# Kernel optimization log

Hardware: AMD Instinct MI355X
Metric: run time of the kernel (lower is better)

The kernel has to match this reference:

```python
import jax, jax.numpy as jnp
import numpy as np

DIM = 512
DIM_TIME = 64
DIM_FF = 2048
B, L = 2, 512
EPS = 1e-5


def _layer_norm(x, g, b):
    mu = jnp.mean(x, axis=-1, keepdims=True)
    var = jnp.mean((x - mu) ** 2, axis=-1, keepdims=True)
    return (x - mu) * jax.lax.rsqrt(var + EPS) * g + b


def _sioconv(u, wa, hid_re, hid_im):
    # u: (B, L, Dt) float. Faithful to the FFT/triu construction, expressed as
    # cumulative log-sums (linear conv with all-ones == causal cumsum).
    Bb, Ll, Dt = u.shape
    out = (u @ wa.T).reshape(Bb, Ll, Dt, 2)          # linear_a, view_as_complex
    a_sqr = out[..., 0] ** 2 + out[..., 1] ** 2
    a = (out[..., 0] + 1j * out[..., 1]) * (jax.lax.rsqrt(a_sqr) * jnp.exp(-a_sqr))
    a = jnp.transpose(a, (0, 2, 1))                  # (B, Dt, L)
    a_ln = jnp.log(a)
    S = jnp.cumsum(a_ln, axis=-1)                    # S_k = sum_{j<=k} ln a_j
    S_prev = jnp.concatenate([jnp.zeros_like(S[..., :1]), S[..., :-1]], axis=-1)
    # c[b,d,i,k] = exp(S_k - S_{i-1}) = prod_{j=i..k} a_j, kept for k >= i-1
    diff = S[:, :, None, :] - S_prev[:, :, :, None]  # (B, Dt, L, L)
    idx = jnp.arange(Ll)
    mask = idx[None, :] >= (idx[:, None] - 1)        # k >= i-1 (triu diag=-1)
    c = jnp.where(mask, jnp.exp(diff), 0.0)
    uc = jnp.transpose(u.astype(jnp.complex64), (0, 2, 1))   # (B, Dt, L)
    hidden = (hid_re + 1j * hid_im)[None, :] * jnp.ones((Bb, 1), jnp.complex64)
    xin = jnp.concatenate([hidden[..., None], uc[..., :-1]], axis=-1)  # rolled + h0
    h = jnp.einsum('bdik,bdk->bdi', c, xin)
    h = h.at[:, :, -1].add(uc[:, :, -1])
    return jnp.transpose(h.real, (0, 2, 1)).astype(u.dtype)


def _ffn(x, w1, b1, w2, b2):
    return jax.nn.silu(x @ w1.T + b1) @ w2.T + b2


def setup_inputs() -> dict:
    key = jax.random.key(0)
    ks = jax.random.split(key, 12)
    d, dt, dff = DIM, DIM_TIME, DIM_FF
    return {
        'x': jax.random.normal(ks[0], (B, L, d), jnp.float32),
        'ln1_g': jnp.ones((d,), jnp.float32), 'ln1_b': jnp.zeros((d,), jnp.float32),
        'fc_w': jax.random.normal(ks[1], (dt, d), jnp.float32) * d ** -0.5,
        'fc_b': jnp.zeros((dt,), jnp.float32),
        'lin_in_w': jax.random.normal(ks[2], (dt, d), jnp.float32) * d ** -0.5,
        'lin_in_b': jnp.zeros((dt,), jnp.float32),
        'wa': jax.random.normal(ks[3], (2 * dt, dt), jnp.float32) * dt ** -0.5,
        'hid_re': jax.random.normal(ks[4], (dt,), jnp.float32),
        'hid_im': jax.random.normal(ks[5], (dt,), jnp.float32),
        'lin_out_w': jax.random.normal(ks[6], (d, dt), jnp.float32) * dt ** -0.5,
        'lin_out_b': jnp.zeros((d,), jnp.float32),
        'ln2_g': jnp.ones((d,), jnp.float32), 'ln2_b': jnp.zeros((d,), jnp.float32),
        'w1': jax.random.normal(ks[7], (dff, d), jnp.float32) * d ** -0.5,
        'b1': jnp.zeros((dff,), jnp.float32),
        'w2': jax.random.normal(ks[8], (d, dff), jnp.float32) * dff ** -0.5,
        'b2': jnp.zeros((d,), jnp.float32),
    }


def reference(x, ln1_g, ln1_b, fc_w, fc_b, lin_in_w, lin_in_b, wa, hid_re, hid_im,
              lin_out_w, lin_out_b, ln2_g, ln2_b, w1, b1, w2, b2):
    x_res = x
    xn = _layer_norm(x, ln1_g, ln1_b)
    y = jax.nn.silu(xn @ fc_w.T + fc_b)                  # gate, (B, L, Dt)
    u = xn @ lin_in_w.T + lin_in_b                       # (B, L, Dt)
    h = _sioconv(u, wa, hid_re, hid_im)
    x = (h * y) @ lin_out_w.T + lin_out_b + x_res        # dropout = identity (eval)
    x_res = x
    x = _ffn(_layer_norm(x, ln2_g, ln2_b), w1, b1, w2, b2) + x_res
    return x
```

## Files before the change

### kernel.cpp

```cpp
#include <hip/hip_runtime.h>
#include <math.h>

#define LSEQ 512
#define DMODEL 512
#define DT 64
#define DFF 2048

typedef unsigned short u16;
typedef __attribute__((ext_vector_type(8))) short short8;
typedef __attribute__((ext_vector_type(4))) float f32x4;
typedef __attribute__((ext_vector_type(16))) float f32x16;

__device__ __forceinline__ float wave_sum(float v) {
#pragma unroll
  for (int o = 32; o > 0; o >>= 1) v += __shfl_xor(v, o, 64);
  return v;
}

__device__ __forceinline__ u16 f2bf(float f) {
  unsigned int u = __float_as_uint(f);
  u += 0x7fffu + ((u >> 16) & 1u);
  return (u16)(u >> 16);
}
__device__ __forceinline__ float bf2f(u16 h) {
  return __uint_as_float(((unsigned int)h) << 16);
}
__device__ __forceinline__ void splitbf(float f, u16& h, u16& l) {
  h = f2bf(f);
  l = f2bf(f - bf2f(h));
}


__global__ __launch_bounds__(256) void k_pre(
    const float* __restrict__ w1, const float* __restrict__ w2,
    const float* __restrict__ fcw, const float* __restrict__ liw,
    const float* __restrict__ wa, const float* __restrict__ low,
    const float* __restrict__ x, const float* __restrict__ g1,
    const float* __restrict__ be1,
    u16* __restrict__ w1s, u16* __restrict__ w2s,
    u16* __restrict__ fclh, u16* __restrict__ fcll,
    u16* __restrict__ wah, u16* __restrict__ wal,
    u16* __restrict__ lowh, u16* __restrict__ lowl,
    u16* __restrict__ xnh, u16* __restrict__ xnl)
{
  if (blockIdx.x >= 2152) {
    const int lane = threadIdx.x & 63, wv = threadIdx.x >> 6;
    const int row = (blockIdx.x - 2152) * 4 + wv;
    const float* xr = x + (size_t)row * DMODEL;
    float v[8]; float s = 0.f;
#pragma unroll
    for (int j = 0; j < 8; ++j) { v[j] = xr[lane + 64 * j]; s += v[j]; }
    s = wave_sum(s);
    const float mu = s * (1.f / 512.f);
    float q = 0.f;
#pragma unroll
    for (int j = 0; j < 8; ++j) { float dd = v[j] - mu; q += dd * dd; }
    q = wave_sum(q);
    const float rstd = rsqrtf(q * (1.f / 512.f) + 1e-5f);
#pragma unroll
    for (int j = 0; j < 8; ++j) {
      int idx = lane + 64 * j;
      float o = (v[j] - mu) * rstd * g1[idx] + be1[idx];
      u16 h, l; splitbf(o, h, l);
      xnh[(size_t)row * DMODEL + idx] = h;
      xnl[(size_t)row * DMODEL + idx] = l;
    }
    return;
  }
  int i = blockIdx.x * 256 + threadIdx.x;
  if (i >= 550912) return;
  if (i < 262144) {
    int r = i >> 7, c0 = (i & 127) << 2;
    float4 v = ((const float4*)w1)[i];
    ushort4 o;
    o.x = f2bf(v.x); o.y = f2bf(v.y); o.z = f2bf(v.z); o.w = f2bf(v.w);
    int lane = (r & 31) + (((c0 & 15) >> 3) << 5);
    int flat = (r >> 5) * 16384 + (c0 >> 4) * 512 + lane * 8 + (c0 & 7);
    *(ushort4*)(w1s + flat) = o;
    return;
  }
  if (i < 524288) {
    int ii = i - 262144;
    int r = ii >> 9, c0 = (ii & 511) << 2;
    float4 v = ((const float4*)w2)[ii];
    ushort4 o;
    o.x = f2bf(v.x); o.y = f2bf(v.y); o.z = f2bf(v.z); o.w = f2bf(v.w);
    int lane = (r & 31) + (((c0 & 15) >> 3) << 5);
    int flat = (r >> 5) * 65536 + (c0 >> 4) * 512 + lane * 8 + (c0 & 7);
    *(ushort4*)(w2s + flat) = o;
    return;
  }
  const float* s; int j; u16 *dh, *dl;
  if (i < 532480)      { s = fcw; j = i - 524288;        dh = fclh; dl = fcll; }
  else if (i < 540672) { s = liw; j = i - 532480 + 8192; dh = fclh; dl = fcll; }
  else if (i < 542720) { s = wa;  j = i - 540672;        dh = wah;  dl = wal;  }
  else                 { s = low; j = i - 542720;        dh = lowh; dl = lowl; }
  int soff = (i < 532480) ? i - 524288 :
             (i < 540672) ? i - 532480 :
             (i < 542720) ? i - 540672 : i - 542720;
  float4 v = ((const float4*)s)[soff];
  ushort4 oh, ol;
  splitbf(v.x, oh.x, ol.x); splitbf(v.y, oh.y, ol.y);
  splitbf(v.z, oh.z, ol.z); splitbf(v.w, oh.w, ol.w);
  ((ushort4*)dh)[j] = oh;
  ((ushort4*)dl)[j] = ol;
}

__global__ __launch_bounds__(512) void k_fa(
    const u16* __restrict__ xnh, const u16* __restrict__ xnl,
    const u16* __restrict__ fclh, const u16* __restrict__ fcll,
    const u16* __restrict__ wah, const u16* __restrict__ wal,
    const float* __restrict__ fcb, const float* __restrict__ lib,
    float* __restrict__ y_o, float* __restrict__ u_o,
    float* __restrict__ ar_o, float* __restrict__ ai_o)
{
  __shared__ __align__(16) u16 ush[16][80];
  __shared__ __align__(16) u16 usl[16][80];
  const int w = threadIdx.x >> 6, lane = threadIdx.x & 63;
  const int mt = blockIdx.x;
  const int lr = lane & 15, lk = lane >> 4;

  {
    const size_t aoff = (size_t)(mt * 16 + lr) * DMODEL + lk * 8;
    const size_t boff = (size_t)(w * 16 + lr) * DMODEL + lk * 8;
    f32x4 acc = {};
#pragma unroll 4
    for (int k = 0; k < DMODEL; k += 32) {
      short8 ah = *(const short8*)(xnh + aoff + k);
      short8 al = *(const short8*)(xnl + aoff + k);
      short8 bh = *(const short8*)(fclh + boff + k);
      short8 bl = *(const short8*)(fcll + boff + k);
      acc = __builtin_amdgcn_mfma_f32_16x16x32_bf16(ah, bh, acc, 0, 0, 0);
      acc = __builtin_amdgcn_mfma_f32_16x16x32_bf16(ah, bl, acc, 0, 0, 0);
      acc = __builtin_amdgcn_mfma_f32_16x16x32_bf16(al, bh, acc, 0, 0, 0);
    }
    const int c = w * 16 + lr;
#pragma unroll
    for (int j = 0; j < 4; ++j) {
      int rl = lk * 4 + j;
      int row = mt * 16 + rl;
      float v = acc[j];
      if (c < DT) {
        v += fcb[c];
        y_o[row * DT + c] = v / (1.f + expf(-v));
      } else {
        int d = c - DT;
        v += lib[d];
        u_o[row * DT + d] = v;
        u16 h, l; splitbf(v, h, l);
        ush[rl][d] = h; usl[rl][d] = l;
      }
    }
  }
  __syncthreads();
  {
    const size_t boff = (size_t)(w * 16 + lr) * DT + lk * 8;
    f32x4 acc = {};
#pragma unroll
    for (int ks = 0; ks < 2; ++ks) {
      short8 ah = *(const short8*)&ush[lr][ks * 32 + lk * 8];
      short8 al = *(const short8*)&usl[lr][ks * 32 + lk * 8];
      short8 bh = *(const short8*)(wah + boff + ks * 32);
      short8 bl = *(const short8*)(wal + boff + ks * 32);
      acc = __builtin_amdgcn_mfma_f32_16x16x32_bf16(ah, bh, acc, 0, 0, 0);
      acc = __builtin_amdgcn_mfma_f32_16x16x32_bf16(ah, bl, acc, 0, 0, 0);
      acc = __builtin_amdgcn_mfma_f32_16x16x32_bf16(al, bh, acc, 0, 0, 0);
    }
    const int c = w * 16 + lr;
#pragma unroll
    for (int j = 0; j < 4; ++j) {
      float v = acc[j];
      float p = __shfl_xor(v, 1, 64);
      float re = (lane & 1) ? p : v;
      float im = (lane & 1) ? v : p;
      float asq = re * re + im * im;
      float sc = rsqrtf(asq) * expf(-asq);
      int row = mt * 16 + lk * 4 + j;
      int d = c >> 1;
      if (lane & 1) ai_o[row * DT + d] = im * sc;
      else          ar_o[row * DT + d] = re * sc;
    }
  }
}

__global__ __launch_bounds__(64) void k_scan2(
    const float* __restrict__ u, const float* __restrict__ ar, const float* __restrict__ ai,
    const float* __restrict__ hr, const float* __restrict__ hi, float* __restrict__ h_o)
{
  const int blk = blockIdx.x;
  const int b = blk >> 6, d = blk & 63;
  const int lane = threadIdx.x;
  const size_t base = (size_t)b * LSEQ * DT + d;
  const int i0 = lane * 8;

  float a_r[8], a_i[8], b_r[8], b_i[8];
#pragma unroll
  for (int e = 0; e < 8; ++e) {
    int i = i0 + e;
    a_r[e] = ar[base + (size_t)i * DT];
    a_i[e] = ai[base + (size_t)i * DT];
    if (i >= 2)      { b_r[e] = u[base + (size_t)(i - 2) * DT]; b_i[e] = 0.f; }
    else if (i == 1) { b_r[e] = hr[d]; b_i[e] = hi[d]; }
    else             { b_r[e] = 0.f;   b_i[e] = 0.f; }
  }

  float Ar = 1.f, Ai = 0.f, Br = 0.f, Bi = 0.f;
#pragma unroll
  for (int e = 0; e < 8; ++e) {
    float nBr = fmaf(Ar, b_r[e], fmaf(-Ai, b_i[e], Br));
    float nBi = fmaf(Ar, b_i[e], fmaf( Ai, b_r[e], Bi));
    float nAr = Ar * a_r[e] - Ai * a_i[e];
    float nAi = Ar * a_i[e] + Ai * a_r[e];
    Ar = nAr; Ai = nAi; Br = nBr; Bi = nBi;
  }

#pragma unroll
  for (int dlt = 1; dlt < 64; dlt <<= 1) {
    float Ar2 = __shfl_down(Ar, dlt, 64);
    float Ai2 = __shfl_down(Ai, dlt, 64);
    float Br2 = __shfl_down(Br, dlt, 64);
    float Bi2 = __shfl_down(Bi, dlt, 64);
    if (lane + dlt < 64) {
      float nAr = Ar * Ar2 - Ai * Ai2;
      float nAi = Ar * Ai2 + Ai * Ar2;
      float nBr = fmaf(Ar, Br2, fmaf(-Ai, Bi2, Br));
      float nBi = fmaf(Ar, Bi2, fmaf( Ai, Br2, Bi));
      Ar = nAr; Ai = nAi; Br = nBr; Bi = nBi;
    }
  }

  float A1r = __shfl_down(Ar, 1, 64), A1i = __shfl_down(Ai, 1, 64);
  float B1r = __shfl_down(Br, 1, 64), B1i = __shfl_down(Bi, 1, 64);
  if (lane == 63) { A1r = 1.f; A1i = 0.f; B1r = 0.f; B1i = 0.f; }
  const float r512 = u[base + (size_t)(LSEQ - 2) * DT];
  float rr = fmaf(A1r, r512, B1r);
  float ri = fmaf(A1i, r512, B1i);

  const float uL = u[base + (size_t)(LSEQ - 1) * DT];
#pragma unroll
  for (int e = 7; e >= 0; --e) {
    int i = i0 + e;
    float nr = fmaf(a_r[e], rr, fmaf(-a_i[e], ri, b_r[e]));
    float ni = fmaf(a_r[e], ri, fmaf( a_i[e], rr, b_i[e]));
    rr = nr; ri = ni;
    float outv = rr;
    if (i == LSEQ - 1) outv += uL;
    h_o[base + (size_t)i * DT] = outv;
  }
}

__global__ __launch_bounds__(1024) void k_midln(
    const float* __restrict__ h, const float* __restrict__ y,
    const u16* __restrict__ lowh, const u16* __restrict__ lowl,
    const float* __restrict__ lob, const float* __restrict__ x,
    const float* __restrict__ g2, const float* __restrict__ be2,
    float* __restrict__ x2_o, u16* __restrict__ xn2s)
{
  __shared__ __align__(16) u16 hyh[16][80];
  __shared__ __align__(16) u16 hyl[16][80];
  __shared__ float x2s[16][520];
  const int tid = threadIdx.x;
  const int w = tid >> 6, lane = tid & 63;
  const int lr = lane & 15, lk = lane >> 4;
  const int mt = blockIdx.x;

  {
    int r = tid >> 6, d = tid & 63;
    int row = mt * 16 + r;
    float v = h[row * DT + d] * y[row * DT + d];
    u16 hh, ll; splitbf(v, hh, ll);
    hyh[r][d] = hh; hyl[r][d] = ll;
  }
  __syncthreads();

#pragma unroll
  for (int t = 0; t < 2; ++t) {
    const int nt = w * 2 + t;
    const size_t boff = (size_t)(nt * 16 + lr) * DT + lk * 8;
    f32x4 acc = {};
#pragma unroll
    for (int ks = 0; ks < 2; ++ks) {
      short8 ah = *(const short8*)&hyh[lr][ks * 32 + lk * 8];
      short8 al = *(const short8*)&hyl[lr][ks * 32 + lk * 8];
      short8 bh = *(const short8*)(lowh + boff + ks * 32);
      short8 bl = *(const short8*)(lowl + boff + ks * 32);
      acc = __builtin_amdgcn_mfma_f32_16x16x32_bf16(ah, bh, acc, 0, 0, 0);
      acc = __builtin_amdgcn_mfma_f32_16x16x32_bf16(ah, bl, acc, 0, 0, 0);
      acc = __builtin_amdgcn_mfma_f32_16x16x32_bf16(al, bh, acc, 0, 0, 0);
    }
    const int c = nt * 16 + lr;
#pragma unroll
    for (int j = 0; j < 4; ++j) {
      int rl = lk * 4 + j;
      int row = mt * 16 + rl;
      float v = acc[j] + lob[c] + x[(size_t)row * DMODEL + c];
      x2s[rl][c] = v;
      x2_o[(size_t)row * DMODEL + c] = v;
    }
  }
  __syncthreads();

  {
    const int r = w;
    const int row = mt * 16 + r;
    float v[8]; float s = 0.f;
#pragma unroll
    for (int j = 0; j < 8; ++j) { v[j] = x2s[r][lane + 64 * j]; s += v[j]; }
    s = wave_sum(s);
    const float mu = s * (1.f / 512.f);
    float q = 0.f;
#pragma unroll
    for (int j = 0; j < 8; ++j) { float dd = v[j] - mu; q += dd * dd; }
    q = wave_sum(q);
    const float rstd = rsqrtf(q * (1.f / 512.f) + 1e-5f);
    const int t32 = row >> 5, r32 = row & 31;
#pragma unroll
    for (int j = 0; j < 8; ++j) {
      int idx = lane + 64 * j;
      float o = (v[j] - mu) * rstd * g2[idx] + be2[idx];
      int lane_s = r32 + (((idx & 15) >> 3) << 5);
      xn2s[t32 * 16384 + (idx >> 4) * 512 + lane_s * 8 + (idx & 7)] = f2bf(o);
    }
  }
}

__global__ __launch_bounds__(256) void k_ffn1(
    const u16* __restrict__ As, const u16* __restrict__ Bs,
    const float* __restrict__ bias, u16* __restrict__ Cs)
{
  const int w = threadIdx.x >> 6, lane = threadIdx.x & 63;
  const int mt = blockIdx.x, nt = blockIdx.y * 4 + w;
  const u16* a = As + mt * 16384 + lane * 8;
  const u16* b = Bs + nt * 16384 + lane * 8;
  f32x16 acc = {};
#pragma unroll 8
  for (int kb = 0; kb < 32; ++kb)
    acc = __builtin_amdgcn_mfma_f32_32x32x16_bf16(*(const short8*)(a + kb * 512),
                                                  *(const short8*)(b + kb * 512),
                                                  acc, 0, 0, 0);
  const int l31 = lane & 31, hi = lane >> 5;
  const int col = nt * 32 + l31;
  const float bb = bias[col];
  const int kb_c = col >> 4;
  const int half_c = (col & 15) >> 3, e_c = col & 7;
#pragma unroll
  for (int r = 0; r < 16; ++r) {
    int row32 = (r & 3) + 8 * (r >> 2) + 4 * hi;
    float v = acc[r] + bb;
    v = v / (1.f + expf(-v));
    int lane_s = row32 + (half_c << 5);
    Cs[mt * 65536 + kb_c * 512 + lane_s * 8 + e_c] = f2bf(v);
  }
}

__global__ __launch_bounds__(256) void k_ffn2(
    const u16* __restrict__ As, const u16* __restrict__ Bs,
    const float* __restrict__ b2, const float* __restrict__ x2,
    float* __restrict__ out)
{
  __shared__ float red[4][16][64];
  const int w = threadIdx.x >> 6, lane = threadIdx.x & 63;
  const int mt = blockIdx.x, nt = blockIdx.y;
  const u16* a = As + mt * 65536 + w * 32 * 512 + lane * 8;
  const u16* b = Bs + nt * 65536 + w * 32 * 512 + lane * 8;
  f32x16 acc = {};
#pragma unroll 8
  for (int kb = 0; kb < 32; ++kb)
    acc = __builtin_amdgcn_mfma_f32_32x32x16_bf16(*(const short8*)(a + kb * 512),
                                                  *(const short8*)(b + kb * 512),
                                                  acc, 0, 0, 0);
#pragma unroll
  for (int r = 0; r < 16; ++r) red[w][r][lane] = acc[r];
  __syncthreads();
  for (int s = threadIdx.x; s < 1024; s += 256) {
    int r = s >> 6, l = s & 63;
    float v = red[0][r][l] + red[1][r][l] + red[2][r][l] + red[3][r][l];
    int row = mt * 32 + (r & 3) + 8 * (r >> 2) + 4 * (l >> 5);
    int col = nt * 32 + (l & 31);
    out[(size_t)row * DMODEL + col] =
        v + b2[col] + x2[(size_t)row * DMODEL + col];
  }
}

extern "C" void kernel_launch(void* const* d_in, const int* in_sizes, int n_in,
                              void* d_out, int out_size, void* d_ws, size_t ws_size,
                              hipStream_t stream) {
  const float* x    = (const float*)d_in[0];
  const float* ln1g = (const float*)d_in[1];
  const float* ln1b = (const float*)d_in[2];
  const float* fcw  = (const float*)d_in[3];
  const float* fcb  = (const float*)d_in[4];
  const float* liw  = (const float*)d_in[5];
  const float* lib  = (const float*)d_in[6];
  const float* wa   = (const float*)d_in[7];
  const float* hidr = (const float*)d_in[8];
  const float* hidi = (const float*)d_in[9];
  const float* low  = (const float*)d_in[10];
  const float* lob  = (const float*)d_in[11];
  const float* ln2g = (const float*)d_in[12];
  const float* ln2b = (const float*)d_in[13];
  const float* w1   = (const float*)d_in[14];
  const float* b1   = (const float*)d_in[15];
  const float* w2   = (const float*)d_in[16];
  const float* b2   = (const float*)d_in[17];
  float* out = (float*)d_out;
  float* ws  = (float*)d_ws;

  float* y_   = ws;
  float* u_   = y_  + 65536;
  float* ar_  = u_  + 65536;
  float* ai_  = ar_ + 65536;
  float* h_   = ai_ + 65536;
  float* x2_  = h_  + 65536;
  u16* p = (u16*)(x2_ + 524288);
  u16* xnh  = p;            p += 524288;
  u16* xnl  = p;            p += 524288;
  u16* xn2s = p;            p += 524288;
  u16* h1s  = p;            p += 2097152;
  u16* w1s  = p;            p += 1048576;
  u16* w2s  = p;            p += 1048576;
  u16* fclh = p;            p += 65536;
  u16* fcll = p;            p += 65536;
  u16* wah  = p;            p += 8192;
  u16* wal  = p;            p += 8192;
  u16* lowh = p;            p += 32768;
  u16* lowl = p;            p += 32768;

  k_pre<<<2408, 256, 0, stream>>>(w1, w2, fcw, liw, wa, low, x, ln1g, ln1b,
                                  w1s, w2s, fclh, fcll, wah, wal, lowh, lowl,
                                  xnh, xnl);
  k_fa<<<64, 512, 0, stream>>>(xnh, xnl, fclh, fcll, wah, wal, fcb, lib,
                               y_, u_, ar_, ai_);
  k_scan2<<<128, 64, 0, stream>>>(u_, ar_, ai_, hidr, hidi, h_);
  k_midln<<<64, 1024, 0, stream>>>(h_, y_, lowh, lowl, lob, x, ln2g, ln2b,
                                   x2_, xn2s);
  k_ffn1<<<dim3(32, 16), 256, 0, stream>>>(xn2s, w1s, b1, h1s);
  k_ffn2<<<dim3(32, 16), 256, 0, stream>>>(h1s, w2s, b2, x2_, out);
}
```

Measured before the change: 62.86 us.

## Fuse all six kernels into one cooperative persistent kernel with grid syncs

Replaces the six separate launches (weight prep/LN1, gate+a projection, scan, out-proj+LN2, FFN1, FFN2) with a single cooperative kernel of 256 blocks of 512 threads. Stages are separated by grid-wide syncs, and per-stage shared memory is overlaid in a union. This removes the per-launch overhead and the inter-kernel gaps. In exchange, several stages now run on only a fraction of the grid (64 blocks or 128 waves), and each grid barrier has its own cost.

Result: slower. 222.9 us (+254.6%).

```diff
diff --git a/kernel.cpp b/kernel.cpp
--- a/kernel.cpp
+++ b/kernel.cpp
@@ -1,5 +1,8 @@
 #include <hip/hip_runtime.h>
+#include <hip/hip_cooperative_groups.h>
 #include <math.h>
+
+namespace cg = cooperative_groups;
 
 #define LSEQ 512
 #define DMODEL 512
@@ -31,21 +34,41 @@
 }
 
 
-__global__ __launch_bounds__(256) void k_pre(
+__global__ __launch_bounds__(512, 2) void k_mega(
     const float* __restrict__ w1, const float* __restrict__ w2,
     const float* __restrict__ fcw, const float* __restrict__ liw,
     const float* __restrict__ wa, const float* __restrict__ low,
     const float* __restrict__ x, const float* __restrict__ g1,
-    const float* __restrict__ be1,
+    const float* __restrict__ be1, const float* __restrict__ fcb,
+    const float* __restrict__ lib, const float* __restrict__ hidr,
+    const float* __restrict__ hidi, const float* __restrict__ lob,
+    const float* __restrict__ g2, const float* __restrict__ be2,
+    const float* __restrict__ b1, const float* __restrict__ b2,
+    float* __restrict__ y_, float* __restrict__ u_,
+    float* __restrict__ ar_, float* __restrict__ ai_,
+    float* __restrict__ h_, float* __restrict__ x2_,
+    u16* __restrict__ xnh, u16* __restrict__ xnl,
+    u16* __restrict__ xn2s, u16* __restrict__ h1s,
     u16* __restrict__ w1s, u16* __restrict__ w2s,
     u16* __restrict__ fclh, u16* __restrict__ fcll,
     u16* __restrict__ wah, u16* __restrict__ wal,
     u16* __restrict__ lowh, u16* __restrict__ lowl,
-    u16* __restrict__ xnh, u16* __restrict__ xnl)
+    float* __restrict__ out)
 {
-  if (blockIdx.x >= 2152) {
-    const int lane = threadIdx.x & 63, wv = threadIdx.x >> 6;
-    const int row = (blockIdx.x - 2152) * 4 + wv;
+  alignas(16) __shared__ union {
+    struct { u16 ush[16][80]; u16 usl[16][80]; } s1;
+    struct { u16 hyh[16][80]; u16 hyl[16][80]; float x2s[16][520]; } s3;
+    struct { float red[2][4][16][64]; } s5;
+  } sm;
+
+  cg::grid_group gg = cg::this_grid();
+  const int blk = blockIdx.x, tid = threadIdx.x;
+  const int wv = tid >> 6, lane = tid & 63;
+  const int gw = blk * 8 + wv;
+  const int lr = lane & 15, lk = lane >> 4;
+
+  if (gw < 1024) {
+    const int row = gw;
     const float* xr = x + (size_t)row * DMODEL;
     float v[8]; float s = 0.f;
 #pragma unroll
@@ -65,320 +88,282 @@
       xnh[(size_t)row * DMODEL + idx] = h;
       xnl[(size_t)row * DMODEL + idx] = l;
     }
-    return;
-  }
-  int i = blockIdx.x * 256 + threadIdx.x;
-  if (i >= 550912) return;
-  if (i < 262144) {
-    int r = i >> 7, c0 = (i & 127) << 2;
-    float4 v = ((const float4*)w1)[i];
-    ushort4 o;
-    o.x = f2bf(v.x); o.y = f2bf(v.y); o.z = f2bf(v.z); o.w = f2bf(v.w);
-    int lane = (r & 31) + (((c0 & 15) >> 3) << 5);
-    int flat = (r >> 5) * 16384 + (c0 >> 4) * 512 + lane * 8 + (c0 & 7);
-    *(ushort4*)(w1s + flat) = o;
-    return;
-  }
-  if (i < 524288) {
-    int ii = i - 262144;
-    int r = ii >> 9, c0 = (ii & 511) << 2;
-    float4 v = ((const float4*)w2)[ii];
-    ushort4 o;
-    o.x = f2bf(v.x); o.y = f2bf(v.y); o.z = f2bf(v.z); o.w = f2bf(v.w);
-    int lane = (r & 31) + (((c0 & 15) >> 3) << 5);
-    int flat = (r >> 5) * 65536 + (c0 >> 4) * 512 + lane * 8 + (c0 & 7);
-    *(ushort4*)(w2s + flat) = o;
-    return;
-  }
-  const float* s; int j; u16 *dh, *dl;
-  if (i < 532480)      { s = fcw; j = i - 524288;        dh = fclh; dl = fcll; }
-  else if (i < 540672) { s = liw; j = i - 532480 + 8192; dh = fclh; dl = fcll; }
-  else if (i < 542720) { s = wa;  j = i - 540672;        dh = wah;  dl = wal;  }
-  else                 { s = low; j = i - 542720;        dh = lowh; dl = lowl; }
-  int soff = (i < 532480) ? i - 524288 :
-             (i < 540672) ? i - 532480 :
-             (i < 542720) ? i - 540672 : i - 542720;
-  float4 v = ((const float4*)s)[soff];
-  ushort4 oh, ol;
-  splitbf(v.x, oh.x, ol.x); splitbf(v.y, oh.y, ol.y);
-  splitbf(v.z, oh.z, ol.z); splitbf(v.w, oh.w, ol.w);
-  ((ushort4*)dh)[j] = oh;
-  ((ushort4*)dl)[j] = ol;
-}
-
-__global__ __launch_bounds__(512) void k_fa(
-    const u16* __restrict__ xnh, const u16* __restrict__ xnl,
-    const u16* __restrict__ fclh, const u16* __restrict__ fcll,
-    const u16* __restrict__ wah, const u16* __restrict__ wal,
-    const float* __restrict__ fcb, const float* __restrict__ lib,
-    float* __restrict__ y_o, float* __restrict__ u_o,
-    float* __restrict__ ar_o, float* __restrict__ ai_o)
-{
-  __shared__ __align__(16) u16 ush[16][80];
-  __shared__ __align__(16) u16 usl[16][80];
-  const int w = threadIdx.x >> 6, lane = threadIdx.x & 63;
-  const int mt = blockIdx.x;
-  const int lr = lane & 15, lk = lane >> 4;
+  }
+  for (int i = blk * 512 + tid; i < 550912; i += 131072) {
+    if (i < 262144) {
+      int r = i >> 7, c0 = (i & 127) << 2;
+      float4 v = ((const float4*)w1)[i];
+      ushort4 o;
+      o.x = f2bf(v.x); o.y = f2bf(v.y); o.z = f2bf(v.z); o.w = f2bf(v.w);
+      int lane_s = (r & 31) + (((c0 & 15) >> 3) << 5);
+      int flat = (r >> 5) * 16384 + (c0 >> 4) * 512 + lane_s * 8 + (c0 & 7);
+      *(ushort4*)(w1s + flat) = o;
+    } else if (i < 524288) {
+      int ii = i - 262144;
+      int r = ii >> 9, c0 = (ii & 511) << 2;
+      float4 v = ((const float4*)w2)[ii];
+      ushort4 o;
+      o.x = f2bf(v.x); o.y = f2bf(v.y); o.z = f2bf(v.z); o.w = f2bf(v.w);
+      int lane_s = (r & 31) + (((c0 & 15) >> 3) << 5);
+      int flat = (r >> 5) * 65536 + (c0 >> 4) * 512 + lane_s * 8 + (c0 & 7);
+      *(ushort4*)(w2s + flat) = o;
+    } else {
+      const float* s; int j; u16 *dh, *dl;
+      if (i < 532480)      { s = fcw; j = i - 524288;        dh = fclh; dl = fcll; }
+      else if (i < 540672) { s = liw; j = i - 532480 + 8192; dh = fclh; dl = fcll; }
+      else if (i < 542720) { s = wa;  j = i - 540672;        dh = wah;  dl = wal;  }
+      else                 { s = low; j = i - 542720;        dh = lowh; dl = lowl; }
+      int soff = (i < 532480) ? i - 524288 :
+                 (i < 540672) ? i - 532480 :
+                 (i < 542720) ? i - 540672 : i - 542720;
+      float4 v = ((const float4*)s)[soff];
+      ushort4 oh, ol;
+      splitbf(v.x, oh.x, ol.x); splitbf(v.y, oh.y, ol.y);
+      splitbf(v.z, oh.z, ol.z); splitbf(v.w, oh.w, ol.w);
+      ((ushort4*)dh)[j] = oh;
+      ((ushort4*)dl)[j] = ol;
+    }
+  }
+  gg.sync();
+
+  if (blk < 64) {
+    const int mt = blk;
+    {
+      const size_t aoff = (size_t)(mt * 16 + lr) * DMODEL + lk * 8;
+      const size_t boff = (size_t)(wv * 16 + lr) * DMODEL + lk * 8;
+      f32x4 acc = {};
+#pragma unroll 4
+      for (int k = 0; k < DMODEL; k += 32) {
+        short8 ah = *(const short8*)(xnh + aoff + k);
+        short8 al = *(const short8*)(xnl + aoff + k);
+        short8 bh = *(const short8*)(fclh + boff + k);
+        short8 bl = *(const short8*)(fcll + boff + k);
+        acc = __builtin_amdgcn_mfma_f32_16x16x32_bf16(ah, bh, acc, 0, 0, 0);
+        acc = __builtin_amdgcn_mfma_f32_16x16x32_bf16(ah, bl, acc, 0, 0, 0);
+        acc = __builtin_amdgcn_mfma_f32_16x16x32_bf16(al, bh, acc, 0, 0, 0);
+      }
+      const int c = wv * 16 + lr;
+#pragma unroll
+      for (int j = 0; j < 4; ++j) {
+        int rl = lk * 4 + j;
+        int row = mt * 16 + rl;
+        float v = acc[j];
+        if (c < DT) {
+          v += fcb[c];
+          y_[row * DT + c] = v / (1.f + expf(-v));
+        } else {
+          int d = c - DT;
+          v += lib[d];
+          u_[row * DT + d] = v;
+          u16 h, l; splitbf(v, h, l);
+          sm.s1.ush[rl][d] = h; sm.s1.usl[rl][d] = l;
+        }
+      }
+    }
+    __syncthreads();
+    {
+      const size_t boff = (size_t)(wv * 16 + lr) * DT + lk * 8;
+      f32x4 acc = {};
+#pragma unroll
+      for (int ks = 0; ks < 2; ++ks) {
+        short8 ah = *(const short8*)&sm.s1.ush[lr][ks * 32 + lk * 8];
+        short8 al = *(const short8*)&sm.s1.usl[lr][ks * 32 + lk * 8];
+        short8 bh = *(const short8*)(wah + boff + ks * 32);
+        short8 bl = *(const short8*)(wal + boff + ks * 32);
+        acc = __builtin_amdgcn_mfma_f32_16x16x32_bf16(ah, bh, acc, 0, 0, 0);
+        acc = __builtin_amdgcn_mfma_f32_16x16x32_bf16(ah, bl, acc, 0, 0, 0);
+        acc = __builtin_amdgcn_mfma_f32_16x16x32_bf16(al, bh, acc, 0, 0, 0);
+      }
+      const int c = wv * 16 + lr;
+#pragma unroll
+      for (int j = 0; j < 4; ++j) {
+        float v = acc[j];
+        float p = __shfl_xor(v, 1, 64);
+        float re = (lane & 1) ? p : v;
+        float im = (lane & 1) ? v : p;
+        float asq = re * re + im * im;
+        float sc = rsqrtf(asq) * expf(-asq);
+        int row = mt * 16 + lk * 4 + j;
+        int d = c >> 1;
+        if (lane & 1) ai_[row * DT + d] = im * sc;
+        else          ar_[row * DT + d] = re * sc;
+      }
+    }
+  }
+  gg.sync();
+
+  if (gw < 128) {
+    const int b = gw >> 6, d = gw & 63;
+    const size_t base = (size_t)b * LSEQ * DT + d;
+    const int i0 = lane * 8;
+    float a_r[8], a_i[8], b_r[8], b_i[8];
+#pragma unroll
+    for (int e = 0; e < 8; ++e) {
+      int i = i0 + e;
+      a_r[e] = ar_[base + (size_t)i * DT];
+      a_i[e] = ai_[base + (size_t)i * DT];
+      if (i >= 2)      { b_r[e] = u_[base + (size_t)(i - 2) * DT]; b_i[e] = 0.f; }
+      else if (i == 1) { b_r[e] = hidr[d]; b_i[e] = hidi[d]; }
+      else             { b_r[e] = 0.f;     b_i[e] = 0.f; }
+    }
+    float Ar = 1.f, Ai = 0.f, Br = 0.f, Bi = 0.f;
+#pragma unroll
+    for (int e = 0; e < 8; ++e) {
+      float nBr = fmaf(Ar, b_r[e], fmaf(-Ai, b_i[e], Br));
+      float nBi = fmaf(Ar, b_i[e], fmaf( Ai, b_r[e], Bi));
+      float nAr = Ar * a_r[e] - Ai * a_i[e];
+      float nAi = Ar * a_i[e] + Ai * a_r[e];
+      Ar = nAr; Ai = nAi; Br = nBr; Bi = nBi;
+    }
+#pragma unroll
+    for (int dlt = 1; dlt < 64; dlt <<= 1) {
+      float Ar2 = __shfl_down(Ar, dlt, 64);
+      float Ai2 = __shfl_down(Ai, dlt, 64);
+      float Br2 = __shfl_down(Br, dlt, 64);
+      float Bi2 = __shfl_down(Bi, dlt, 64);
+      if (lane + dlt < 64) {
+        float nAr = Ar * Ar2 - Ai * Ai2;
+        float nAi = Ar * Ai2 + Ai * Ar2;
+        float nBr = fmaf(Ar, Br2, fmaf(-Ai, Bi2, Br));
+        float nBi = fmaf(Ar, Bi2, fmaf( Ai, Br2, Bi));
+        Ar = nAr; Ai = nAi; Br = nBr; Bi = nBi;
+      }
+    }
+    float A1r = __shfl_down(Ar, 1, 64), A1i = __shfl_down(Ai, 1, 64);
+    float B1r = __shfl_down(Br, 1, 64), B1i = __shfl_down(Bi, 1, 64);
+    if (lane == 63) { A1r = 1.f; A1i = 0.f; B1r = 0.f; B1i = 0.f; }
+    const float r512 = u_[base + (size_t)(LSEQ - 2) * DT];
+    float rr = fmaf(A1r, r512, B1r);
+    float ri = fmaf(A1i, r512, B1i);
+    const float uL = u_[base + (size_t)(LSEQ - 1) * DT];
+#pragma unroll
+    for (int e = 7; e >= 0; --e) {
+      int i = i0 + e;
+      float nr = fmaf(a_r[e], rr, fmaf(-a_i[e], ri, b_r[e]));
+      float ni = fmaf(a_r[e], ri, fmaf( a_i[e], rr, b_i[e]));
+      rr = nr; ri = ni;
+      float outv = rr;
+      if (i == LSEQ - 1) outv += uL;
+      h_[base + (size_t)i * DT] = outv;
+    }
+  }
+  gg.sync();
+
+  if (blk < 64) {
+    const int mt = blk;
+#pragma unroll
+    for (int it = 0; it < 2; ++it) {
+      int idx = it * 512 + tid;
+      int r = idx >> 6, d = idx & 63;
+      int row = mt * 16 + r;
+      float v = h_[row * DT + d] * y_[row * DT + d];
+      u16 hh, ll; splitbf(v, hh, ll);
+      sm.s3.hyh[r][d] = hh; sm.s3.hyl[r][d] = ll;
+    }
+    __syncthreads();
+#pragma unroll
+    for (int t = 0; t < 4; ++t) {
+      const int nt = wv * 4 + t;
+      const size_t boff = (size_t)(nt * 16 + lr) * DT + lk * 8;
+      f32x4 acc = {};
+#pragma unroll
+      for (int ks = 0; ks < 2; ++ks) {
+        short8 ah = *(const short8*)&sm.s3.hyh[lr][ks * 32 + lk * 8];
+        short8 al = *(const short8*)&sm.s3.hyl[lr][ks * 32 + lk * 8];
+        short8 bh = *(const short8*)(lowh + boff + ks * 32);
+        short8 bl = *(const short8*)(lowl + boff + ks * 32);
+        acc = __builtin_amdgcn_mfma_f32_16x16x32_bf16(ah, bh, acc, 0, 0, 0);
+        acc = __builtin_amdgcn_mfma_f32_16x16x32_bf16(ah, bl, acc, 0, 0, 0);
+        acc = __builtin_amdgcn_mfma_f32_16x16x32_bf16(al, bh, acc, 0, 0, 0);
+      }
+      const int c = nt * 16 + lr;
+#pragma unroll
+      for (int j = 0; j < 4; ++j) {
+        int rl = lk * 4 + j;
+        int row = mt * 16 + rl;
+        float v = acc[j] + lob[c] + x[(size_t)row * DMODEL + c];
+        sm.s3.x2s[rl][c] = v;
+        x2_[(size_t)row * DMODEL + c] = v;
+      }
+    }
+    __syncthreads();
+#pragma unroll
+    for (int rr2 = 0; rr2 < 2; ++rr2) {
+      const int r = wv * 2 + rr2;
+      const int row = mt * 16 + r;
+      float v[8]; float s = 0.f;
+#pragma unroll
+      for (int j = 0; j < 8; ++j) { v[j] = sm.s3.x2s[r][lane + 64 * j]; s += v[j]; }
+      s = wave_sum(s);
+      const float mu = s * (1.f / 512.f);
+      float q = 0.f;
+#pragma unroll
+      for (int j = 0; j < 8; ++j) { float dd = v[j] - mu; q += dd * dd; }
+      q = wave_sum(q);
+      const float rstd = rsqrtf(q * (1.f / 512.f) + 1e-5f);
+      const int t32 = row >> 5, r32 = row & 31;
+#pragma unroll
+      for (int j = 0; j < 8; ++j) {
+        int idx = lane + 64 * j;
+        float o = (v[j] - mu) * rstd * g2[idx] + be2[idx];
+        int lane_s = r32 + (((idx & 15) >> 3) << 5);
+        xn2s[t32 * 16384 + (idx >> 4) * 512 + lane_s * 8 + (idx & 7)] = f2bf(o);
+      }
+    }
+  }
+  gg.sync();
 
   {
-    const size_t aoff = (size_t)(mt * 16 + lr) * DMODEL + lk * 8;
-    const size_t boff = (size_t)(w * 16 + lr) * DMODEL + lk * 8;
-    f32x4 acc = {};
-#pragma unroll 4
-    for (int k = 0; k < DMODEL; k += 32) {
-      short8 ah = *(const short8*)(xnh + aoff + k);
-      short8 al = *(const short8*)(xnl + aoff + k);
-      short8 bh = *(const short8*)(fclh + boff + k);
-      short8 bl = *(const short8*)(fcll + boff + k);
-      acc = __builtin_amdgcn_mfma_f32_16x16x32_bf16(ah, bh, acc, 0, 0, 0);
-      acc = __builtin_amdgcn_mfma_f32_16x16x32_bf16(ah, bl, acc, 0, 0, 0);
-      acc = __builtin_amdgcn_mfma_f32_16x16x32_bf16(al, bh, acc, 0, 0, 0);
-    }
-    const int c = w * 16 + lr;
-#pragma unroll
-    for (int j = 0; j < 4; ++j) {
-      int rl = lk * 4 + j;
-      int row = mt * 16 + rl;
-      float v = acc[j];
-      if (c < DT) {
-        v += fcb[c];
-        y_o[row * DT + c] = v / (1.f + expf(-v));
-      } else {
-        int d = c - DT;
-        v += lib[d];
-        u_o[row * DT + d] = v;
-        u16 h, l; splitbf(v, h, l);
-        ush[rl][d] = h; usl[rl][d] = l;
-      }
-    }
-  }
-  __syncthreads();
+    const int mt = gw & 31, nt = gw >> 5;
+    const u16* a = xn2s + mt * 16384 + lane * 8;
+    const u16* b = w1s + nt * 16384 + lane * 8;
+    f32x16 acc = {};
+#pragma unroll 8
+    for (int kb = 0; kb < 32; ++kb)
+      acc = __builtin_amdgcn_mfma_f32_32x32x16_bf16(*(const short8*)(a + kb * 512),
+                                                    *(const short8*)(b + kb * 512),
+                                                    acc, 0, 0, 0);
+    const int l31 = lane & 31, hi = lane >> 5;
+    const int col = nt * 32 + l31;
+    const float bb = b1[col];
+    const int kb_c = col >> 4;
+    const int half_c = (col & 15) >> 3, e_c = col & 7;
+#pragma unroll
+    for (int r = 0; r < 16; ++r) {
+      int row32 = (r & 3) + 8 * (r >> 2) + 4 * hi;
+      float v = acc[r] + bb;
+      v = v / (1.f + expf(-v));
+      int lane_s = row32 + (half_c << 5);
+      h1s[mt * 65536 + kb_c * 512 + lane_s * 8 + e_c] = f2bf(v);
+    }
+  }
+  gg.sync();
+
   {
-    const size_t boff = (size_t)(w * 16 + lr) * DT + lk * 8;
-    f32x4 acc = {};
-#pragma unroll
-    for (int ks = 0; ks < 2; ++ks) {
-      short8 ah = *(const short8*)&ush[lr][ks * 32 + lk * 8];
-      short8 al = *(const short8*)&usl[lr][ks * 32 + lk * 8];
-      short8 bh = *(const short8*)(wah + boff + ks * 32);
-      short8 bl = *(const short8*)(wal + boff + ks * 32);
-      acc = __builtin_amdgcn_mfma_f32_16x16x32_bf16(ah, bh, acc, 0, 0, 0);
-      acc = __builtin_amdgcn_mfma_f32_16x16x32_bf16(ah, bl, acc, 0, 0, 0);
-      acc = __builtin_amdgcn_mfma_f32_16x16x32_bf16(al, bh, acc, 0, 0, 0);
-    }
-    const int c = w * 16 + lr;
-#pragma unroll
-    for (int j = 0; j < 4; ++j) {
-      float v = acc[j];
-      float p = __shfl_xor(v, 1, 64);
-      float re = (lane & 1) ? p : v;
-      float im = (lane & 1) ? v : p;
-      float asq = re * re + im * im;
-      float sc = rsqrtf(asq) * expf(-asq);
-      int row = mt * 16 + lk * 4 + j;
-      int d = c >> 1;
-      if (lane & 1) ai_o[row * DT + d] = im * sc;
-      else          ar_o[row * DT + d] = re * sc;
-    }
-  }
-}
-
-__global__ __launch_bounds__(64) void k_scan2(
-    const float* __restrict__ u, const float* __restrict__ ar, const float* __restrict__ ai,
-    const float* __restrict__ hr, const float* __restrict__ hi, float* __restrict__ h_o)
-{
-  const int blk = blockIdx.x;
-  const int b = blk >> 6, d = blk & 63;
-  const int lane = threadIdx.x;
-  const size_t base = (size_t)b * LSEQ * DT + d;
-  const int i0 = lane * 8;
-
-  float a_r[8], a_i[8], b_r[8], b_i[8];
-#pragma unroll
-  for (int e = 0; e < 8; ++e) {
-    int i = i0 + e;
-    a_r[e] = ar[base + (size_t)i * DT];
-    a_i[e] = ai[base + (size_t)i * DT];
-    if (i >= 2)      { b_r[e] = u[base + (size_t)(i - 2) * DT]; b_i[e] = 0.f; }
-    else if (i == 1) { b_r[e] = hr[d]; b_i[e] = hi[d]; }
-    else             { b_r[e] = 0.f;   b_i[e] = 0.f; }
-  }
-
-  float Ar = 1.f, Ai = 0.f, Br = 0.f, Bi = 0.f;
-#pragma unroll
-  for (int e = 0; e < 8; ++e) {
-    float nBr = fmaf(Ar, b_r[e], fmaf(-Ai, b_i[e], Br));
-    float nBi = fmaf(Ar, b_i[e], fmaf( Ai, b_r[e], Bi));
-    float nAr = Ar * a_r[e] - Ai * a_i[e];
-    float nAi = Ar * a_i[e] + Ai * a_r[e];
-    Ar = nAr; Ai = nAi; Br = nBr; Bi = nBi;
-  }
-
-#pragma unroll
-  for (int dlt = 1; dlt < 64; dlt <<= 1) {
-    float Ar2 = __shfl_down(Ar, dlt, 64);
-    float Ai2 = __shfl_down(Ai, dlt, 64);
-    float Br2 = __shfl_down(Br, dlt, 64);
-    float Bi2 = __shfl_down(Bi, dlt, 64);
-    if (lane + dlt < 64) {
-      float nAr = Ar * Ar2 - Ai * Ai2;
-      float nAi = Ar * Ai2 + Ai * Ar2;
-      float nBr = fmaf(Ar, Br2, fmaf(-Ai, Bi2, Br));
-      float nBi = fmaf(Ar, Bi2, fmaf( Ai, Br2, Bi));
-      Ar = nAr; Ai = nAi; Br = nBr; Bi = nBi;
-    }
-  }
-
-  float A1r = __shfl_down(Ar, 1, 64), A1i = __shfl_down(Ai, 1, 64);
-  float B1r = __shfl_down(Br, 1, 64), B1i = __shfl_down(Bi, 1, 64);
-  if (lane == 63) { A1r = 1.f; A1i = 0.f; B1r = 0.f; B1i = 0.f; }
-  const float r512 = u[base + (size_t)(LSEQ - 2) * DT];
-  float rr = fmaf(A1r, r512, B1r);
-  float ri = fmaf(A1i, r512, B1i);
-
-  const float uL = u[base + (size_t)(LSEQ - 1) * DT];
-#pragma unroll
-  for (int e = 7; e >= 0; --e) {
-    int i = i0 + e;
-    float nr = fmaf(a_r[e], rr, fmaf(-a_i[e], ri, b_r[e]));
-    float ni = fmaf(a_r[e], ri, fmaf( a_i[e], rr, b_i[e]));
-    rr = nr; ri = ni;
-    float outv = rr;
-    if (i == LSEQ - 1) outv += uL;
-    h_o[base + (size_t)i * DT] = outv;
-  }
-}
-
-__global__ __launch_bounds__(1024) void k_midln(
-    const float* __restrict__ h, const float* __restrict__ y,
-    const u16* __restrict__ lowh, const u16* __restrict__ lowl,
-    const float* __restrict__ lob, const float* __restrict__ x,
-    const float* __restrict__ g2, const float* __restrict__ be2,
-    float* __restrict__ x2_o, u16* __restrict__ xn2s)
-{
-  __shared__ __align__(16) u16 hyh[16][80];
-  __shared__ __align__(16) u16 hyl[16][80];
-  __shared__ float x2s[16][520];
-  const int tid = threadIdx.x;
-  const int w = tid >> 6, lane = tid & 63;
-  const int lr = lane & 15, lk = lane >> 4;
-  const int mt = blockIdx.x;
-
-  {
-    int r = tid >> 6, d = tid & 63;
-    int row = mt * 16 + r;
-    float v = h[row * DT + d] * y[row * DT + d];
-    u16 hh, ll; splitbf(v, hh, ll);
-    hyh[r][d] = hh; hyl[r][d] = ll;
-  }
-  __syncthreads();
-
-#pragma unroll
-  for (int t = 0; t < 2; ++t) {
-    const int nt = w * 2 + t;
-    const size_t boff = (size_t)(nt * 16 + lr) * DT + lk * 8;
-    f32x4 acc = {};
-#pragma unroll
-    for (int ks = 0; ks < 2; ++ks) {
-      short8 ah = *(const short8*)&hyh[lr][ks * 32 + lk * 8];
-      short8 al = *(const short8*)&hyl[lr][ks * 32 + lk * 8];
-      short8 bh = *(const short8*)(lowh + boff + ks * 32);
-      short8 bl = *(const short8*)(lowl + boff + ks * 32);
-      acc = __builtin_amdgcn_mfma_f32_16x16x32_bf16(ah, bh, acc, 0, 0, 0);
-      acc = __builtin_amdgcn_mfma_f32_16x16x32_bf16(ah, bl, acc, 0, 0, 0);
-      acc = __builtin_amdgcn_mfma_f32_16x16x32_bf16(al, bh, acc, 0, 0, 0);
-    }
-    const int c = nt * 16 + lr;
-#pragma unroll
-    for (int j = 0; j < 4; ++j) {
-      int rl = lk * 4 + j;
-      int row = mt * 16 + rl;
-      float v = acc[j] + lob[c] + x[(size_t)row * DMODEL + c];
-      x2s[rl][c] = v;
-      x2_o[(size_t)row * DMODEL + c] = v;
-    }
-  }
-  __syncthreads();
-
-  {
-    const int r = w;
-    const int row = mt * 16 + r;
-    float v[8]; float s = 0.f;
-#pragma unroll
-    for (int j = 0; j < 8; ++j) { v[j] = x2s[r][lane + 64 * j]; s += v[j]; }
-    s = wave_sum(s);
-    const float mu = s * (1.f / 512.f);
-    float q = 0.f;
-#pragma unroll
-    for (int j = 0; j < 8; ++j) { float dd = v[j] - mu; q += dd * dd; }
-    q = wave_sum(q);
-    const float rstd = rsqrtf(q * (1.f / 512.f) + 1e-5f);
-    const int t32 = row >> 5, r32 = row & 31;
-#pragma unroll
-    for (int j = 0; j < 8; ++j) {
-      int idx = lane + 64 * j;
-      float o = (v[j] - mu) * rstd * g2[idx] + be2[idx];
-      int lane_s = r32 + (((idx & 15) >> 3) << 5);
-      xn2s[t32 * 16384 + (idx >> 4) * 512 + lane_s * 8 + (idx & 7)] = f2bf(o);
-    }
-  }
-}
-
-__global__ __launch_bounds__(256) void k_ffn1(
-    const u16* __restrict__ As, const u16* __restrict__ Bs,
-    const float* __restrict__ bias, u16* __restrict__ Cs)
-{
-  const int w = threadIdx.x >> 6, lane = threadIdx.x & 63;
-  const int mt = blockIdx.x, nt = blockIdx.y * 4 + w;
-  const u16* a = As + mt * 16384 + lane * 8;
-  const u16* b = Bs + nt * 16384 + lane * 8;
-  f32x16 acc = {};
+    const int sub = wv >> 2, wq = wv & 3;
+    const int ti = blk * 2 + sub;
+    const int mt = ti & 31, nt = ti >> 5;
+    const u16* a = h1s + mt * 65536 + wq * 16384 + lane * 8;
+    const u16* b = w2s + nt * 65536 + wq * 16384 + lane * 8;
+    f32x16 acc = {};
 #pragma unroll 8
-  for (int kb = 0; kb < 32; ++kb)
-    acc = __builtin_amdgcn_mfma_f32_32x32x16_bf16(*(const short8*)(a + kb * 512),
-                                                  *(const short8*)(b + kb * 512),
-                                                  acc, 0, 0, 0);
-  const int l31 = lane & 31, hi = lane >> 5;
-  const int col = nt * 32 + l31;
-  const float bb = bias[col];
-  const int kb_c = col >> 4;
-  const int half_c = (col & 15) >> 3, e_c = col & 7;
-#pragma unroll
-  for (int r = 0; r < 16; ++r) {
-    int row32 = (r & 3) + 8 * (r >> 2) + 4 * hi;
-    float v = acc[r] + bb;
-    v = v / (1.f + expf(-v));
-    int lane_s = row32 + (half_c << 5);
-    Cs[mt * 65536 + kb_c * 512 + lane_s * 8 + e_c] = f2bf(v);
-  }
-}
-
-__global__ __launch_bounds__(256) void k_ffn2(
-    const u16* __restrict__ As, const u16* __restrict__ Bs,
-    const float* __restrict__ b2, const float* __restrict__ x2,
-    float* __restrict__ out)
-{
-  __shared__ float red[4][16][64];
-  const int w = threadIdx.x >> 6, lane = threadIdx.x & 63;
-  const int mt = blockIdx.x, nt = blockIdx.y;
-  const u16* a = As + mt * 65536 + w * 32 * 512 + lane * 8;
-  const u16* b = Bs + nt * 65536 + w * 32 * 512 + lane * 8;
-  f32x16 acc = {};
-#pragma unroll 8
-  for (int kb = 0; kb < 32; ++kb)
-    acc = __builtin_amdgcn_mfma_f32_32x32x16_bf16(*(const short8*)(a + kb * 512),
-                                                  *(const short8*)(b + kb * 512),
-                                                  acc, 0, 0, 0);
-#pragma unroll
-  for (int r = 0; r < 16; ++r) red[w][r][lane] = acc[r];
-  __syncthreads();
-  for (int s = threadIdx.x; s < 1024; s += 256) {
-    int r = s >> 6, l = s & 63;
-    float v = red[0][r][l] + red[1][r][l] + red[2][r][l] + red[3][r][l];
-    int row = mt * 32 + (r & 3) + 8 * (r >> 2) + 4 * (l >> 5);
-    int col = nt * 32 + (l & 31);
-    out[(size_t)row * DMODEL + col] =
-        v + b2[col] + x2[(size_t)row * DMODEL + col];
+    for (int kb = 0; kb < 32; ++kb)
+      acc = __builtin_amdgcn_mfma_f32_32x32x16_bf16(*(const short8*)(a + kb * 512),
+                                                    *(const short8*)(b + kb * 512),
+                                                    acc, 0, 0, 0);
+#pragma unroll
+    for (int r = 0; r < 16; ++r) sm.s5.red[sub][wq][r][lane] = acc[r];
+    __syncthreads();
+    const int tloc = wq * 64 + lane;
+    for (int s = tloc; s < 1024; s += 256) {
+      int r = s >> 6, l = s & 63;
+      float v = sm.s5.red[sub][0][r][l] + sm.s5.red[sub][1][r][l] +
+                sm.s5.red[sub][2][r][l] + sm.s5.red[sub][3][r][l];
+      int row = mt * 32 + (r & 3) + 8 * (r >> 2) + 4 * (l >> 5);
+      int col = nt * 32 + (l & 31);
+      out[(size_t)row * DMODEL + col] =
+          v + b2[col] + x2_[(size_t)row * DMODEL + col];
+    }
   }
 }
 
@@ -426,14 +411,17 @@
   u16* lowh = p;            p += 32768;
   u16* lowl = p;            p += 32768;
 
-  k_pre<<<2408, 256, 0, stream>>>(w1, w2, fcw, liw, wa, low, x, ln1g, ln1b,
-                                  w1s, w2s, fclh, fcll, wah, wal, lowh, lowl,
-                                  xnh, xnl);
-  k_fa<<<64, 512, 0, stream>>>(xnh, xnl, fclh, fcll, wah, wal, fcb, lib,
-                               y_, u_, ar_, ai_);
-  k_scan2<<<128, 64, 0, stream>>>(u_, ar_, ai_, hidr, hidi, h_);
-  k_midln<<<64, 1024, 0, stream>>>(h_, y_, lowh, lowl, lob, x, ln2g, ln2b,
-                                   x2_, xn2s);
-  k_ffn1<<<dim3(32, 16), 256, 0, stream>>>(xn2s, w1s, b1, h1s);
-  k_ffn2<<<dim3(32, 16), 256, 0, stream>>>(h1s, w2s, b2, x2_, out);
-}
+  void* kp[] = {
+    (void*)&w1, (void*)&w2, (void*)&fcw, (void*)&liw, (void*)&wa, (void*)&low,
+    (void*)&x, (void*)&ln1g, (void*)&ln1b, (void*)&fcb, (void*)&lib,
+    (void*)&hidr, (void*)&hidi, (void*)&lob, (void*)&ln2g, (void*)&ln2b,
+    (void*)&b1, (void*)&b2,
+    (void*)&y_, (void*)&u_, (void*)&ar_, (void*)&ai_, (void*)&h_, (void*)&x2_,
+    (void*)&xnh, (void*)&xnl, (void*)&xn2s, (void*)&h1s,
+    (void*)&w1s, (void*)&w2s, (void*)&fclh, (void*)&fcll,
+    (void*)&wah, (void*)&wal, (void*)&lowh, (void*)&lowl,
+    (void*)&out
+  };
+  hipLaunchCooperativeKernel((const void*)k_mega, dim3(256), dim3(512),
+                             kp, 0, stream);
+}
```
